# Kernel optimization log

Hardware: AMD Instinct MI355X
Metric: run time of the kernel (lower is better)

## Reference

```python
import jax, jax.numpy as jnp
import numpy as np

N_NODES = 8192
N_EDGES = 65536
NB = 10            # number_of_basis
MID = 32           # middle_layer_size
MAX_R = 10.0       # max_radius
NZ, NM = 48, 16    # z / mol embedding sizes -> 64x0e node input
IN_S = NZ + NM     # 64 scalars
H_S, H_V = 32, 8   # hidden irreps 32x0e + 8x1o (dim 56)
O_S = 16           # output irreps 16x0e
W0N = IN_S * H_S + IN_S * H_V                                  # 2560
W1N = H_S*H_S + H_V*H_S + H_S*H_V + H_V*H_V + H_V*H_V          # 1664
W2N = H_S*O_S + H_V*O_S                                        # 640
H_DIM = H_S + 3 * H_V                                          # 56


def _fcnet(e, W1, W2):
    # e3nn FullyConnectedNet([NB, MID, numel], silu): fan-in normalized linears
    h = jax.nn.silu(e @ W1 / np.sqrt(W1.shape[0]))
    return h @ W2 / np.sqrt(W2.shape[0])


def _ln(x, g, b):
    m = jnp.mean(x, -1, keepdims=True)
    v = jnp.var(x, -1, keepdims=True)
    return (x - m) * jax.lax.rsqrt(v + 1e-5) * g + b


def _sus(t):
    # smooth compact-support bump helper: exp(-1/t) for t>0 else 0
    return jnp.where(t > 0, jnp.exp(-1.0 / jnp.where(t > 0, t, 1.0)), 0.0)


def _forward(pos, Ez, Em,
             b0_W1, b0_W2, b0_g, b0_b,
             b1_W1, b1_W2, b1_g, b1_b,
             b2_W1, b2_W2, b2_g, b2_b,
             z, mol_id, edge_src, edge_dst):
    N = pos.shape[0]
    E = edge_src.shape[0]
    avg = E / N  # avg_num_neighbors (static)

    # node embedding: 64x0e
    x = jnp.concatenate([Ez[z], Em[mol_id]], axis=-1)          # [N, 64]

    vec = pos[edge_dst] - pos[edge_src]                        # [E, 3]
    length = jnp.linalg.norm(vec, axis=1)                      # [E]

    # soft_one_hot_linspace(basis='smooth_finite', cutoff=True) * sqrt(NB)
    vals = jnp.linspace(0.0, MAX_R, NB + 2)[1:-1]
    step = MAX_R / (NB + 1)
    u = (length[:, None] - vals) / step
    emb = (1.14136 * np.exp(2.0)) * _sus(u + 1.0) * _sus(1.0 - u)
    emb = emb * np.sqrt(NB)                                    # [E, NB]

    # spherical harmonics lmax=1, normalize=True, 'component' norm
    nrm = vec / jnp.maximum(length, 1e-9)[:, None]
    sh_v = np.sqrt(3.0) * nrm                                  # [E, 3]  (l=1; l=0 comp == 1)

    # ---- interaction block 0: 64x0e -> 32x0e + 8x1o ----
    w = _fcnet(emb, b0_W1, b0_W2)                              # [E, 2560]
    w00 = w[:, :IN_S * H_S].reshape(E, IN_S, H_S)
    w01 = w[:, IN_S * H_S:].reshape(E, IN_S, H_V)
    xe = x[edge_src]                                           # [E, 64]
    es = jnp.einsum('eu,euw->ew', xe, w00) / np.sqrt(IN_S)
    ev = jnp.einsum('eu,euw,ei->ewi', xe, w01, sh_v) / np.sqrt(IN_S)
    msg = jnp.concatenate([es, ev.reshape(E, 3 * H_V)], -1)    # [E, 56]
    x = _ln(jax.ops.segment_sum(msg, edge_dst, num_segments=N) / np.sqrt(avg), b0_g, b0_b)

    # ---- interaction block 1: 32x0e+8x1o -> 32x0e+8x1o ----
    w = _fcnet(emb, b1_W1, b1_W2)                              # [E, 1664]
    o = 0
    w_ss  = w[:, o:o + H_S*H_S].reshape(E, H_S, H_S); o += H_S*H_S
    w_vvs = w[:, o:o + H_V*H_S].reshape(E, H_V, H_S); o += H_V*H_S
    w_sv  = w[:, o:o + H_S*H_V].reshape(E, H_S, H_V); o += H_S*H_V
    w_vs  = w[:, o:o + H_V*H_V].reshape(E, H_V, H_V); o += H_V*H_V
    w_vvv = w[:, o:o + H_V*H_V].reshape(E, H_V, H_V)
    xs = x[:, :H_S][edge_src]                                  # [E, 32]
    xv = x[:, H_S:].reshape(N, H_V, 3)[edge_src]               # [E, 8, 3]
    dot = jnp.einsum('eui,ei->eu', xv, sh_v) / np.sqrt(3.0)    # 1o x 1o -> 0e CG
    crs = jnp.cross(xv, sh_v[:, None, :]) / np.sqrt(2.0)       # 1o x 1o -> 1o CG
    es = (jnp.einsum('eu,euw->ew', xs, w_ss) / np.sqrt(H_S)
          + jnp.einsum('eu,euw->ew', dot, w_vvs) / np.sqrt(H_V)) / np.sqrt(2.0)
    ev = (jnp.einsum('eu,euw,ei->ewi', xs, w_sv, sh_v) / np.sqrt(H_S)
          + jnp.einsum('eui,euw->ewi', xv, w_vs) / np.sqrt(H_V)
          + jnp.einsum('eui,euw->ewi', crs, w_vvv) / np.sqrt(H_V)) / np.sqrt(3.0)
    msg = jnp.concatenate([es, ev.reshape(E, 3 * H_V)], -1)
    x = _ln(jax.ops.segment_sum(msg, edge_dst, num_segments=N) / np.sqrt(avg), b1_g, b1_b)

    # ---- interaction block 2: 32x0e+8x1o -> 16x0e ----
    w = _fcnet(emb, b2_W1, b2_W2)                              # [E, 640]
    w_ss  = w[:, :H_S * O_S].reshape(E, H_S, O_S)
    w_vvs = w[:, H_S * O_S:].reshape(E, H_V, O_S)
    xs = x[:, :H_S][edge_src]
    xv = x[:, H_S:].reshape(N, H_V, 3)[edge_src]
    dot = jnp.einsum('eui,ei->eu', xv, sh_v) / np.sqrt(3.0)
    es = (jnp.einsum('eu,euw->ew', xs, w_ss) / np.sqrt(H_S)
          + jnp.einsum('eu,euw->ew', dot, w_vvs) / np.sqrt(H_V)) / np.sqrt(2.0)
    x = _ln(jax.ops.segment_sum(es, edge_dst, num_segments=N) / np.sqrt(avg), b2_g, b2_b)
    return x                                                   # [N, 16]


def setup_inputs():
    key = jax.random.key(0)
    ks = jax.random.split(key, 16)
    edge_src = jax.random.randint(ks[3], (N_EDGES,), 0, N_NODES)
    # exclude self-loops (radius_graph never returns them)
    edge_dst = (edge_src + 1 + jax.random.randint(ks[4], (N_EDGES,), 0, N_NODES - 1)) % N_NODES
    return {
        'pos': jax.random.uniform(ks[0], (N_NODES, 3), jnp.float32) * 8.0,
        'z': jax.random.randint(ks[1], (N_NODES,), 0, 100),
        'mol_id': jax.random.randint(ks[2], (N_NODES,), 0, 2),
        'edge_src': edge_src,
        'edge_dst': edge_dst,
        'Ez': jax.random.normal(ks[5], (100, NZ), jnp.float32),
        'Em': jax.random.normal(ks[6], (2, NM), jnp.float32),
        'b0_W1': jax.random.normal(ks[7], (NB, MID), jnp.float32),
        'b0_W2': jax.random.normal(ks[8], (MID, W0N), jnp.float32),
        'b0_g': jnp.ones((H_DIM,), jnp.float32),
        'b0_b': jnp.zeros((H_DIM,), jnp.float32),
        'b1_W1': jax.random.normal(ks[9], (NB, MID), jnp.float32),
        'b1_W2': jax.random.normal(ks[10], (MID, W1N), jnp.float32),
        'b1_g': jnp.ones((H_DIM,), jnp.float32),
        'b1_b': jnp.zeros((H_DIM,), jnp.float32),
        'b2_W1': jax.random.normal(ks[11], (NB, MID), jnp.float32),
        'b2_W2': jax.random.normal(ks[12], (MID, W2N), jnp.float32),
        'b2_g': jnp.ones((O_S,), jnp.float32),
        'b2_b': jnp.zeros((O_S,), jnp.float32),
    }


def reference(pos, z, mol_id, edge_src, edge_dst, Ez, Em,
              b0_W1, b0_W2, b0_g, b0_b,
              b1_W1, b1_W2, b1_g, b1_b,
              b2_W1, b2_W2, b2_g, b2_b):
    return _forward(pos, Ez, Em,
                    b0_W1, b0_W2, b0_g, b0_b,
                    b1_W1, b1_W2, b1_g, b1_b,
                    b2_W1, b2_W2, b2_g, b2_b,
                    z, mol_id, edge_src, edge_dst)
```

## Files before the change

kernel.cpp:

```cpp
#include <hip/hip_runtime.h>

#define NNODES 8192
#define NEDGES 65536

#define K_PACK   0.02209708691f
#define K_P1SV   0.01804219593f
#define K_VVS    0.04419417382f
#define K_VS     0.03608439182f
#define K_VVV    0.02551551815f
#define K_DOT    0.57735026919f
#define K_PRELN  0.35355339059f
#define C_EMB    8.4335730689f

typedef unsigned int uint32;
typedef unsigned short ushort16;
typedef __attribute__((ext_vector_type(8))) short short8;
typedef __attribute__((ext_vector_type(4))) float floatx4;

__device__ __forceinline__ float siluf(float x) { return x / (1.0f + __expf(-x)); }
__device__ __forceinline__ float susf(float t) { return t > 0.0f ? __expf(-1.0f / t) : 0.0f; }
__device__ __forceinline__ ushort16 f2bf(float f) {
  uint32 u = __float_as_uint(f);
  return (ushort16)((u + 0x7fffu + ((u >> 16) & 1u)) >> 16);
}
__device__ __forceinline__ float bflo(uint32 v) { return __uint_as_float(v << 16); }
__device__ __forceinline__ float bfhi(uint32 v) { return __uint_as_float(v & 0xffff0000u); }
__device__ __forceinline__ float bfs(ushort16 v) { return __uint_as_float((uint32)v << 16); }

__device__ __forceinline__ void mlp32(const float* __restrict__ W, const float emb[10],
                                      float* __restrict__ H) {
#pragma unroll
  for (int m = 0; m < 32; ++m) {
    float t = 0.f;
#pragma unroll
    for (int k = 0; k < 10; ++k) t += emb[k] * W[k * 32 + m];
    H[m] = siluf(t);
  }
}

__global__ __launch_bounds__(256) void k_prep(
    const float* __restrict__ pos, const int* __restrict__ z, const int* __restrict__ mol,
    const int* __restrict__ esrc, const int* __restrict__ edst,
    const float* __restrict__ Ez, const float* __restrict__ Em,
    const float* __restrict__ W10, const float* __restrict__ W11, const float* __restrict__ W12,
    const float* __restrict__ W20, const float* __restrict__ W21, const float* __restrict__ W22,
    int* __restrict__ combo, ushort16* __restrict__ X0cb, float* __restrict__ sh,
    ushort16* __restrict__ h0b, ushort16* __restrict__ h1b, ushort16* __restrict__ h2b,
    ushort16* __restrict__ Bp0, ushort16* __restrict__ Bp1, ushort16* __restrict__ Bp2,
    ushort16* __restrict__ Bpw1, ushort16* __restrict__ Bpw2,
    int* __restrict__ deg, int* __restrict__ eidx) {
  int idx = blockIdx.x * 256 + threadIdx.x;
  if (idx < NEDGES) {
    int e = idx;
    int s = esrc[e], d = edst[e];
    int p = atomicAdd(&deg[d], 1);
    if (p < 64) eidx[(size_t)d * 64 + p] = e;
    float vx = pos[d * 3 + 0] - pos[s * 3 + 0];
    float vy = pos[d * 3 + 1] - pos[s * 3 + 1];
    float vz = pos[d * 3 + 2] - pos[s * 3 + 2];
    float len = sqrtf(vx * vx + vy * vy + vz * vz);
    float inv = 1.7320508076f / fmaxf(len, 1e-9f);
    sh[e * 3 + 0] = vx * inv; sh[e * 3 + 1] = vy * inv; sh[e * 3 + 2] = vz * inv;
    float emb[10];
#pragma unroll
    for (int k = 0; k < 10; ++k) {
      float u = len * 1.1f - (float)(k + 1);
      emb[k] = C_EMB * susf(u + 1.0f) * susf(1.0f - u);
    }
    float H[32];
    uint32* hp;
    mlp32(W10, emb, H);
    hp = (uint32*)(h0b + (size_t)e * 32);
#pragma unroll
    for (int m = 0; m < 16; ++m)
      hp[m] = (uint32)f2bf(H[2 * m]) | ((uint32)f2bf(H[2 * m + 1]) << 16);
    mlp32(W11, emb, H);
    hp = (uint32*)(h1b + (size_t)e * 32);
#pragma unroll
    for (int m = 0; m < 16; ++m)
      hp[m] = (uint32)f2bf(H[2 * m]) | ((uint32)f2bf(H[2 * m + 1]) << 16);
    mlp32(W12, emb, H);
    hp = (uint32*)(h2b + (size_t)e * 32);
#pragma unroll
    for (int m = 0; m < 16; ++m)
      hp[m] = (uint32)f2bf(H[2 * m]) | ((uint32)f2bf(H[2 * m + 1]) << 16);
    return;
  }
  idx -= NEDGES;
  if (idx < NNODES) { combo[idx] = z[idx] * 2 + mol[idx]; return; }
  idx -= NNODES;
  if (idx < 16384) {
    int c = idx >> 6, j = idx & 63;
    float v = 0.f;
    if (c < 200) {
      int zz = c >> 1, mm = c & 1;
      v = (j < 48) ? Ez[zz * 48 + j] : Em[mm * 16 + (j - 48)];
    }
    X0cb[idx] = f2bf(v);
    return;
  }
  idx -= 16384;
  if (idx < 81920) {
    int tile = idx >> 10; int r = idx & 1023;
    int kh = r >> 9; int rr = r & 511;
    int lane = rr >> 3, j = rr & 7;
    int k = kh * 32 + (lane >> 4) * 8 + j;
    int n = tile * 16 + (lane & 15);
    int c = n >> 5, m = n & 31;
    int col = (c < 32) ? (k * 32 + c) : (2048 + k * 8 + (c - 32));
    Bp0[idx] = f2bf(W20[m * 2560 + col] * K_PACK);
    return;
  }
  idx -= 81920;
  if (idx < 40960) {
    int tile = idx >> 9; int rr = idx & 511;
    int lane = rr >> 3, j = rr & 7;
    int k = (lane >> 4) * 8 + j;
    int n = tile * 16 + (lane & 15);
    int c = n >> 5, m = n & 31;
    float v = (c < 32) ? W21[m * 1664 + k * 32 + c] * K_PACK
                       : W21[m * 1664 + 1280 + k * 8 + (c - 32)] * K_P1SV;
    Bp1[idx] = f2bf(v);
    return;
  }
  idx -= 40960;
  if (idx < 16384) {
    int tile = idx >> 9; int rr = idx & 511;
    int lane = rr >> 3, j = rr & 7;
    int k = (lane >> 4) * 8 + j;
    int n = tile * 16 + (lane & 15);
    int c = n >> 5, m = n & 31;
    Bp2[idx] = f2bf(W22[m * 640 + k * 16 + c] * K_PACK);
    return;
  }
  idx -= 16384;
  if (idx < 12288) {
    int tile = idx >> 9; int rr = idx & 511;
    int lane = rr >> 3, j = rr & 7;
    int m = (lane >> 4) * 8 + j;
    int c = tile * 16 + (lane & 15);
    float v;
    if (c < 256) {
      int u = c >> 5, w = c & 31;
      v = W21[m * 1664 + 1024 + u * 32 + w] * K_VVS;
    } else {
      int r2 = c - 256; int t = r2 & 1; int l2 = r2 >> 1;
      int u = l2 >> 3, vv = l2 & 7;
      v = (t == 0) ? W21[m * 1664 + 1536 + u * 8 + vv] * K_VS
                   : W21[m * 1664 + 1600 + u * 8 + vv] * K_VVV;
    }
    Bpw1[idx] = f2bf(v);
    return;
  }
  idx -= 12288;
  {
    int tile = idx >> 9; int rr = idx & 511;
    int lane = rr >> 3, j = rr & 7;
    int m = (lane >> 4) * 8 + j;
    int c = tile * 16 + (lane & 15);
    int t = c & 1; int l2 = c >> 1;
    int u = l2 >> 3, wh = l2 & 7;
    Bpw2[idx] = f2bf(W22[m * 640 + 512 + u * 16 + wh * 2 + t] * K_VVS);
  }
}

__device__ __forceinline__ void gemm_tile(
    const ushort16* __restrict__ A, const ushort16* __restrict__ Bp, ushort16* __restrict__ C,
    int N, int K, int bx, int by, int wave, int lane) {
  int m0 = bx * 64 + wave * 16;
  int n0 = by * 64;
  int row = lane & 15, q = lane >> 4;
  int nkh = K >> 5;
  floatx4 acc[4];
  floatx4 zero = {0.f, 0.f, 0.f, 0.f};
#pragma unroll
  for (int t = 0; t < 4; ++t) acc[t] = zero;
  for (int kh = 0; kh < nkh; ++kh) {
    short8 a = *reinterpret_cast<const short8*>(A + (size_t)(m0 + row) * K + kh * 32 + q * 8);
#pragma unroll
    for (int t = 0; t < 4; ++t) {
      int T = (n0 >> 4) + t;
      short8 b = *reinterpret_cast<const short8*>(Bp + ((size_t)T * nkh + kh) * 512 + lane * 8);
      acc[t] = __builtin_amdgcn_mfma_f32_16x16x32_bf16(a, b, acc[t], 0, 0, 0);
    }
  }
  int colb = n0 + row;
#pragma unroll
  for (int t = 0; t < 4; ++t)
#pragma unroll
    for (int r = 0; r < 4; ++r)
      C[(size_t)(m0 + q * 4 + r) * N + colb + t * 16] = f2bf(acc[t][r]);
}

__global__ __launch_bounds__(256) void k_gemm_mfma(
    const ushort16* __restrict__ A, const ushort16* __restrict__ Bp, ushort16* __restrict__ C,
    int N, int K) {
  gemm_tile(A, Bp, C, N, K, blockIdx.x, blockIdx.y, threadIdx.x >> 6, threadIdx.x & 63);
}

__global__ __launch_bounds__(256) void k_gemm3(
    const ushort16* __restrict__ A0, const ushort16* __restrict__ B0, ushort16* __restrict__ C0,
    int N0, int K0, int nbx0, int nb0,
    const ushort16* __restrict__ A1, const ushort16* __restrict__ B1, ushort16* __restrict__ C1,
    int N1, int K1, int nbx1, int nb1,
    const ushort16* __restrict__ A2, const ushort16* __restrict__ B2, ushort16* __restrict__ C2,
    int N2, int K2, int nbx2) {
  int b = blockIdx.x;
  int wave = threadIdx.x >> 6, lane = threadIdx.x & 63;
  if (b < nb0) {
    gemm_tile(A0, B0, C0, N0, K0, b % nbx0, b / nbx0, wave, lane);
  } else if (b < nb0 + nb1) {
    b -= nb0;
    gemm_tile(A1, B1, C1, N1, K1, b % nbx1, b / nbx1, wave, lane);
  } else {
    b -= nb0 + nb1;
    gemm_tile(A2, B2, C2, N2, K2, b % nbx2, b / nbx2, wave, lane);
  }
}

__global__ __launch_bounds__(256) void k_msg0(
    const int* __restrict__ rowmap, const int* __restrict__ esrc,
    const float* __restrict__ sh, const ushort16* __restrict__ hb,
    const ushort16* __restrict__ Pb, ushort16* __restrict__ msg) {
  int e = __builtin_amdgcn_readfirstlane(blockIdx.x * 4 + (threadIdx.x >> 6));
  int lane = threadIdx.x & 63;
  int s = esrc[e];
  int row = rowmap[s];
  float sh0 = sh[e * 3 + 0], sh1 = sh[e * 3 + 1], sh2 = sh[e * 3 + 2];
  int c; float mult;
  if (lane < 32) { c = lane; mult = 1.0f; }
  else if (lane < 56) {
    int l = lane - 32; int v = l / 3; int i = l - v * 3;
    c = 32 + v;
    mult = (i == 0) ? sh0 : (i == 1 ? sh1 : sh2);
  } else { c = 0; mult = 0.0f; }
  const uint4* Hp = reinterpret_cast<const uint4*>(hb + (size_t)e * 32);
  const uint4* Pp = reinterpret_cast<const uint4*>(Pb + (size_t)row * 1280 + c * 32);
  float a = 0.f;
#pragma unroll
  for (int qq = 0; qq < 4; ++qq) {
    uint4 pv = Pp[qq];
    uint4 hv = Hp[qq];
    a += bflo(pv.x) * bflo(hv.x) + bfhi(pv.x) * bfhi(hv.x);
    a += bflo(pv.y) * bflo(hv.y) + bfhi(pv.y) * bfhi(hv.y);
    a += bflo(pv.z) * bflo(hv.z) + bfhi(pv.z) * bfhi(hv.z);
    a += bflo(pv.w) * bflo(hv.w) + bfhi(pv.w) * bfhi(hv.w);
  }
  if (lane < 56) msg[(size_t)e * 56 + lane] = f2bf(a * mult);
}

__global__ __launch_bounds__(256) void k_msg1(
    const int* __restrict__ esrc, const float* __restrict__ sh, const ushort16* __restrict__ hb,
    const ushort16* __restrict__ Pb, const float* __restrict__ xv,
    const ushort16* __restrict__ Wedge, ushort16* __restrict__ msg) {
  __shared__ float vbuf[4][56];
  int w = threadIdx.x >> 6;
  int e = __builtin_amdgcn_readfirstlane(blockIdx.x * 4 + w);
  int lane = threadIdx.x & 63;
  int s = esrc[e];
  float sh0 = sh[e * 3 + 0], sh1 = sh[e * 3 + 1], sh2 = sh[e * 3 + 2];
  int u = lane >> 3;
  const float* xvp = xv + (size_t)s * 24 + u * 3;
  float x0 = xvp[0], x1 = xvp[1], x2 = xvp[2];
  float du = K_DOT * (x0 * sh0 + x1 * sh1 + x2 * sh2);
  float cr0 = x1 * sh2 - x2 * sh1;
  float cr1 = x2 * sh0 - x0 * sh2;
  float cr2 = x0 * sh1 - x1 * sh0;
  const ushort16* wp = Wedge + (size_t)e * 384;
  uint2 wv = *reinterpret_cast<const uint2*>(wp + lane * 4);
  uint32 wsv = *reinterpret_cast<const uint32*>(wp + 256 + lane * 2);
  float b0 = du * bflo(wv.x), b1 = du * bfhi(wv.x);
  float b2 = du * bflo(wv.y), b3 = du * bfhi(wv.y);
  float avs = bflo(wsv), avv = bfhi(wsv);
  float e0v = x0 * avs + cr0 * avv;
  float e1v = x1 * avs + cr1 * avv;
  float e2v = x2 * avs + cr2 * avv;
#pragma unroll
  for (int off = 8; off < 64; off <<= 1) {
    b0 += __shfl_xor(b0, off, 64); b1 += __shfl_xor(b1, off, 64);
    b2 += __shfl_xor(b2, off, 64); b3 += __shfl_xor(b3, off, 64);
    e0v += __shfl_xor(e0v, off, 64); e1v += __shfl_xor(e1v, off, 64);
    e2v += __shfl_xor(e2v, off, 64);
  }
  if (lane < 8) {
    vbuf[w][lane * 4 + 0] = b0; vbuf[w][lane * 4 + 1] = b1;
    vbuf[w][lane * 4 + 2] = b2; vbuf[w][lane * 4 + 3] = b3;
    vbuf[w][32 + lane * 3 + 0] = e0v;
    vbuf[w][32 + lane * 3 + 1] = e1v;
    vbuf[w][32 + lane * 3 + 2] = e2v;
  }
  int c; float mult;
  if (lane < 32) { c = lane; mult = 1.0f; }
  else if (lane < 56) {
    int l = lane - 32; int v = l / 3; int i = l - v * 3;
    c = 32 + v;
    mult = (i == 0) ? sh0 : (i == 1 ? sh1 : sh2);
  } else { c = 0; mult = 0.0f; }
  const uint4* Hp = reinterpret_cast<const uint4*>(hb + (size_t)e * 32);
  const uint4* Pp = reinterpret_cast<const uint4*>(Pb + (size_t)s * 1280 + c * 32);
  float a = 0.f;
#pragma unroll
  for (int qq = 0; qq < 4; ++qq) {
    uint4 pv = Pp[qq];
    uint4 hv = Hp[qq];
    a += bflo(pv.x) * bflo(hv.x) + bfhi(pv.x) * bfhi(hv.x);
    a += bflo(pv.y) * bflo(hv.y) + bfhi(pv.y) * bfhi(hv.y);
    a += bflo(pv.z) * bflo(hv.z) + bfhi(pv.z) * bfhi(hv.z);
    a += bflo(pv.w) * bflo(hv.w) + bfhi(pv.w) * bfhi(hv.w);
  }
  __syncthreads();
  if (lane < 56) msg[(size_t)e * 56 + lane] = f2bf(a * mult + vbuf[w][lane]);
}

__global__ __launch_bounds__(256) void k_msg2(
    const int* __restrict__ esrc, const float* __restrict__ sh, const ushort16* __restrict__ hb,
    const ushort16* __restrict__ Pb, const float* __restrict__ xv,
    const ushort16* __restrict__ Wedge, ushort16* __restrict__ msg) {
  __shared__ float vbuf[4][16];
  int w = threadIdx.x >> 6;
  int e = __builtin_amdgcn_readfirstlane(blockIdx.x * 4 + w);
  int lane = threadIdx.x & 63;
  int s = esrc[e];
  float sh0 = sh[e * 3 + 0], sh1 = sh[e * 3 + 1], sh2 = sh[e * 3 + 2];
  int u = lane >> 3;
  const float* xvp = xv + (size_t)s * 24 + u * 3;
  float du = K_DOT * (xvp[0] * sh0 + xvp[1] * sh1 + xvp[2] * sh2);
  uint32 w2 = *reinterpret_cast<const uint32*>(Wedge + (size_t)e * 128 + lane * 2);
  float c0 = du * bflo(w2), c1 = du * bfhi(w2);
#pragma unroll
  for (int off = 8; off < 64; off <<= 1) {
    c0 += __shfl_xor(c0, off, 64); c1 += __shfl_xor(c1, off, 64);
  }
  if (lane < 8) { vbuf[w][lane * 2 + 0] = c0; vbuf[w][lane * 2 + 1] = c1; }
  int q = lane >> 4, wc = lane & 15;
  uint4 hv = reinterpret_cast<const uint4*>(hb + (size_t)e * 32)[q];
  uint4 pv = reinterpret_cast<const uint4*>(Pb + (size_t)s * 512 + wc * 32)[q];
  float a = bflo(pv.x) * bflo(hv.x) + bfhi(pv.x) * bfhi(hv.x)
          + bflo(pv.y) * bflo(hv.y) + bfhi(pv.y) * bfhi(hv.y)
          + bflo(pv.z) * bflo(hv.z) + bfhi(pv.z) * bfhi(hv.z)
          + bflo(pv.w) * bflo(hv.w) + bfhi(pv.w) * bfhi(hv.w);
  a += __shfl_xor(a, 16, 64);
  a += __shfl_xor(a, 32, 64);
  __syncthreads();
  if (lane < 16) msg[(size_t)e * 16 + lane] = f2bf(a + vbuf[w][lane]);
}

__global__ __launch_bounds__(256) void k_gather_ln(
    const int* __restrict__ deg, const int* __restrict__ eidx,
    const ushort16* __restrict__ msg, int D,
    const float* __restrict__ g, const float* __restrict__ b,
    ushort16* __restrict__ xsb, float* __restrict__ xvf, float* __restrict__ outf) {
  int n = __builtin_amdgcn_readfirstlane(blockIdx.x * 4 + (threadIdx.x >> 6));
  int lane = threadIdx.x & 63;
  int cnt = deg[n]; if (cnt > 64) cnt = 64;
  const int* ep = eidx + (size_t)n * 64;
  float v = 0.f;
  for (int j = 0; j < cnt; ++j) {
    int e = ep[j];
    if (lane < D) v += bfs(msg[(size_t)e * D + lane]);
  }
  v *= K_PRELN;
  if (lane >= D) v = 0.f;
  float sm = v, sq = v * v;
#pragma unroll
  for (int off = 32; off > 0; off >>= 1) {
    sm += __shfl_xor(sm, off, 64);
    sq += __shfl_xor(sq, off, 64);
  }
  float invD = 1.0f / (float)D;
  float mean = sm * invD;
  float var = sq * invD - mean * mean;
  float rs = rsqrtf(var + 1e-5f);
  float r = (v - mean) * rs * g[lane < D ? lane : 0] + b[lane < D ? lane : 0];
  if (outf) {
    if (lane < D) outf[(size_t)n * D + lane] = r;
  } else {
    if (lane < 32) xsb[(size_t)n * 32 + lane] = f2bf(r);
    else if (lane < 56) xvf[(size_t)n * 24 + lane - 32] = r;
  }
}

extern "C" void kernel_launch(void* const* d_in, const int* in_sizes, int n_in,
                              void* d_out, int out_size, void* d_ws, size_t ws_size,
                              hipStream_t stream) {
  const float* pos = (const float*)d_in[0];
  const int* z = (const int*)d_in[1];
  const int* mol = (const int*)d_in[2];
  const int* esrc = (const int*)d_in[3];
  const int* edst = (const int*)d_in[4];
  const float* Ez = (const float*)d_in[5];
  const float* Em = (const float*)d_in[6];
  const float* b0W1 = (const float*)d_in[7];
  const float* b0W2 = (const float*)d_in[8];
  const float* b0g = (const float*)d_in[9];
  const float* b0b = (const float*)d_in[10];
  const float* b1W1 = (const float*)d_in[11];
  const float* b1W2 = (const float*)d_in[12];
  const float* b1g = (const float*)d_in[13];
  const float* b1b = (const float*)d_in[14];
  const float* b2W1 = (const float*)d_in[15];
  const float* b2W2 = (const float*)d_in[16];
  const float* b2g = (const float*)d_in[17];
  const float* b2b = (const float*)d_in[18];
  float* out = (float*)d_out;

  float* ws = (float*)d_ws;
  size_t o = 0;
  int* combo = (int*)(ws + o); o += NNODES;
  int* deg = (int*)(ws + o); o += NNODES;
  int* eidx = (int*)(ws + o); o += (size_t)NNODES * 64;
  ushort16* X0cb = (ushort16*)(ws + o); o += 8192;
  ushort16* xs1b = (ushort16*)(ws + o); o += 131072;
  float* xv1 = ws + o; o += (size_t)NNODES * 24;
  ushort16* h0b = (ushort16*)(ws + o); o += (size_t)NEDGES * 16;
  ushort16* h1b = (ushort16*)(ws + o); o += (size_t)NEDGES * 16;
  ushort16* h2b = (ushort16*)(ws + o); o += (size_t)NEDGES * 16;
  float* shb = ws + o; o += (size_t)NEDGES * 3;
  ushort16* Bp0 = (ushort16*)(ws + o); o += 40960;
  ushort16* Bp1 = (ushort16*)(ws + o); o += 20480;
  ushort16* Bp2 = (ushort16*)(ws + o); o += 8192;
  ushort16* Bpw1 = (ushort16*)(ws + o); o += 6144;
  ushort16* Bpw2 = (ushort16*)(ws + o); o += 2048;
  ushort16* Wedge1 = (ushort16*)(ws + o); o += (size_t)NEDGES * 192;
  ushort16* Wedge2 = (ushort16*)(ws + o); o += (size_t)NEDGES * 64;
  ushort16* P12 = (ushort16*)(ws + o); o += (size_t)NNODES * 640;
  ushort16* msgb = (ushort16*)(ws + o); o += (size_t)NEDGES * 28;

  ushort16* P0c = P12;
  ushort16* xs2b = xs1b;
  float* xv2 = xv1;
  ushort16* msg16 = msgb;

  hipMemsetAsync(deg, 0, NNODES * sizeof(int), stream);

  k_prep<<<960, 256, 0, stream>>>(pos, z, mol, esrc, edst, Ez, Em,
                                  b0W1, b1W1, b2W1, b0W2, b1W2, b2W2,
                                  combo, X0cb, shb, h0b, h1b, h2b,
                                  Bp0, Bp1, Bp2, Bpw1, Bpw2, deg, eidx);

  k_gemm3<<<8272, 256, 0, stream>>>(h1b, Bpw1, Wedge1, 384, 32, 1024, 6144,
                                    h2b, Bpw2, Wedge2, 128, 32, 1024, 2048,
                                    X0cb, Bp0, P0c, 1280, 64, 4);

  k_msg0<<<16384, 256, 0, stream>>>(combo, esrc, shb, h0b, P0c, msgb);
  k_gather_ln<<<2048, 256, 0, stream>>>(deg, eidx, msgb, 56, b0g, b0b, xs1b, xv1, nullptr);

  k_gemm_mfma<<<dim3(128, 20), 256, 0, stream>>>(xs1b, Bp1, P12, 1280, 32);
  k_msg1<<<16384, 256, 0, stream>>>(esrc, shb, h1b, P12, xv1, Wedge1, msgb);
  k_gather_ln<<<2048, 256, 0, stream>>>(deg, eidx, msgb, 56, b1g, b1b, xs2b, xv2, nullptr);

  k_gemm_mfma<<<dim3(128, 8), 256, 0, stream>>>(xs2b, Bp2, P12, 512, 32);
  k_msg2<<<16384, 256, 0, stream>>>(esrc, shb, h2b, P12, xv2, Wedge2, msg16);
  k_gather_ln<<<2048, 256, 0, stream>>>(deg, eidx, msg16, 16, b2g, b2b, nullptr, nullptr, out);
}
```

Before: 245.9 us.

## Fuse per-edge weight GEMMs into message kernels via MFMA into LDS

```diff
diff --git a/kernel.cpp b/kernel.cpp
--- a/kernel.cpp
+++ b/kernel.cpp
@@ -198,26 +198,6 @@
   gemm_tile(A, Bp, C, N, K, blockIdx.x, blockIdx.y, threadIdx.x >> 6, threadIdx.x & 63);
 }
 
-__global__ __launch_bounds__(256) void k_gemm3(
-    const ushort16* __restrict__ A0, const ushort16* __restrict__ B0, ushort16* __restrict__ C0,
-    int N0, int K0, int nbx0, int nb0,
-    const ushort16* __restrict__ A1, const ushort16* __restrict__ B1, ushort16* __restrict__ C1,
-    int N1, int K1, int nbx1, int nb1,
-    const ushort16* __restrict__ A2, const ushort16* __restrict__ B2, ushort16* __restrict__ C2,
-    int N2, int K2, int nbx2) {
-  int b = blockIdx.x;
-  int wave = threadIdx.x >> 6, lane = threadIdx.x & 63;
-  if (b < nb0) {
-    gemm_tile(A0, B0, C0, N0, K0, b % nbx0, b / nbx0, wave, lane);
-  } else if (b < nb0 + nb1) {
-    b -= nb0;
-    gemm_tile(A1, B1, C1, N1, K1, b % nbx1, b / nbx1, wave, lane);
-  } else {
-    b -= nb0 + nb1;
-    gemm_tile(A2, B2, C2, N2, K2, b % nbx2, b / nbx2, wave, lane);
-  }
-}
-
 __global__ __launch_bounds__(256) void k_msg0(
     const int* __restrict__ rowmap, const int* __restrict__ esrc,
     const float* __restrict__ sh, const ushort16* __restrict__ hb,
@@ -249,100 +229,134 @@
   if (lane < 56) msg[(size_t)e * 56 + lane] = f2bf(a * mult);
 }
 
-__global__ __launch_bounds__(256) void k_msg1(
+__global__ __launch_bounds__(256) void k_msg1f(
     const int* __restrict__ esrc, const float* __restrict__ sh, const ushort16* __restrict__ hb,
     const ushort16* __restrict__ Pb, const float* __restrict__ xv,
-    const ushort16* __restrict__ Wedge, ushort16* __restrict__ msg) {
+    const ushort16* __restrict__ Bpw, ushort16* __restrict__ msg) {
+  __shared__ ushort16 Wlds[16][384];
   __shared__ float vbuf[4][56];
-  int w = threadIdx.x >> 6;
-  int e = __builtin_amdgcn_readfirstlane(blockIdx.x * 4 + w);
-  int lane = threadIdx.x & 63;
-  int s = esrc[e];
-  float sh0 = sh[e * 3 + 0], sh1 = sh[e * 3 + 1], sh2 = sh[e * 3 + 2];
+  int w = threadIdx.x >> 6, lane = threadIdx.x & 63;
+  int e0 = __builtin_amdgcn_readfirstlane(blockIdx.x * 16);
+  int row = lane & 15, q = lane >> 4;
+  short8 a1 = *reinterpret_cast<const short8*>(hb + (size_t)(e0 + row) * 32 + q * 8);
+  floatx4 zero = {0.f, 0.f, 0.f, 0.f};
+#pragma unroll
+  for (int t6 = 0; t6 < 6; ++t6) {
+    int T = w * 6 + t6;
+    short8 b1 = *reinterpret_cast<const short8*>(Bpw + (size_t)T * 512 + lane * 8);
+    floatx4 acc = __builtin_amdgcn_mfma_f32_16x16x32_bf16(a1, b1, zero, 0, 0, 0);
+#pragma unroll
+    for (int r = 0; r < 4; ++r)
+      Wlds[q * 4 + r][T * 16 + row] = f2bf(acc[r]);
+  }
+  __syncthreads();
   int u = lane >> 3;
-  const float* xvp = xv + (size_t)s * 24 + u * 3;
-  float x0 = xvp[0], x1 = xvp[1], x2 = xvp[2];
-  float du = K_DOT * (x0 * sh0 + x1 * sh1 + x2 * sh2);
-  float cr0 = x1 * sh2 - x2 * sh1;
-  float cr1 = x2 * sh0 - x0 * sh2;
-  float cr2 = x0 * sh1 - x1 * sh0;
-  const ushort16* wp = Wedge + (size_t)e * 384;
-  uint2 wv = *reinterpret_cast<const uint2*>(wp + lane * 4);
-  uint32 wsv = *reinterpret_cast<const uint32*>(wp + 256 + lane * 2);
-  float b0 = du * bflo(wv.x), b1 = du * bfhi(wv.x);
-  float b2 = du * bflo(wv.y), b3 = du * bfhi(wv.y);
-  float avs = bflo(wsv), avv = bfhi(wsv);
-  float e0v = x0 * avs + cr0 * avv;
-  float e1v = x1 * avs + cr1 * avv;
-  float e2v = x2 * avs + cr2 * avv;
-#pragma unroll
-  for (int off = 8; off < 64; off <<= 1) {
-    b0 += __shfl_xor(b0, off, 64); b1 += __shfl_xor(b1, off, 64);
-    b2 += __shfl_xor(b2, off, 64); b3 += __shfl_xor(b3, off, 64);
-    e0v += __shfl_xor(e0v, off, 64); e1v += __shfl_xor(e1v, off, 64);
-    e2v += __shfl_xor(e2v, off, 64);
-  }
-  if (lane < 8) {
-    vbuf[w][lane * 4 + 0] = b0; vbuf[w][lane * 4 + 1] = b1;
-    vbuf[w][lane * 4 + 2] = b2; vbuf[w][lane * 4 + 3] = b3;
-    vbuf[w][32 + lane * 3 + 0] = e0v;
-    vbuf[w][32 + lane * 3 + 1] = e1v;
-    vbuf[w][32 + lane * 3 + 2] = e2v;
-  }
-  int c; float mult;
-  if (lane < 32) { c = lane; mult = 1.0f; }
-  else if (lane < 56) {
-    int l = lane - 32; int v = l / 3; int i = l - v * 3;
-    c = 32 + v;
-    mult = (i == 0) ? sh0 : (i == 1 ? sh1 : sh2);
-  } else { c = 0; mult = 0.0f; }
-  const uint4* Hp = reinterpret_cast<const uint4*>(hb + (size_t)e * 32);
-  const uint4* Pp = reinterpret_cast<const uint4*>(Pb + (size_t)s * 1280 + c * 32);
-  float a = 0.f;
-#pragma unroll
-  for (int qq = 0; qq < 4; ++qq) {
-    uint4 pv = Pp[qq];
-    uint4 hv = Hp[qq];
-    a += bflo(pv.x) * bflo(hv.x) + bfhi(pv.x) * bfhi(hv.x);
-    a += bflo(pv.y) * bflo(hv.y) + bfhi(pv.y) * bfhi(hv.y);
-    a += bflo(pv.z) * bflo(hv.z) + bfhi(pv.z) * bfhi(hv.z);
-    a += bflo(pv.w) * bflo(hv.w) + bfhi(pv.w) * bfhi(hv.w);
-  }
-  __syncthreads();
-  if (lane < 56) msg[(size_t)e * 56 + lane] = f2bf(a * mult + vbuf[w][lane]);
-}
-
-__global__ __launch_bounds__(256) void k_msg2(
+#pragma unroll
+  for (int k = 0; k < 4; ++k) {
+    int e = e0 + w * 4 + k;
+    int s = esrc[e];
+    float sh0 = sh[e * 3 + 0], sh1 = sh[e * 3 + 1], sh2 = sh[e * 3 + 2];
+    const float* xvp = xv + (size_t)s * 24 + u * 3;
+    float x0 = xvp[0], x1 = xvp[1], x2 = xvp[2];
+    float du = K_DOT * (x0 * sh0 + x1 * sh1 + x2 * sh2);
+    float cr0 = x1 * sh2 - x2 * sh1;
+    float cr1 = x2 * sh0 - x0 * sh2;
+    float cr2 = x0 * sh1 - x1 * sh0;
+    const ushort16* wp = &Wlds[w * 4 + k][0];
+    uint2 wv = *reinterpret_cast<const uint2*>(wp + lane * 4);
+    uint32 wsv = *reinterpret_cast<const uint32*>(wp + 256 + lane * 2);
+    float b0 = du * bflo(wv.x), b1 = du * bfhi(wv.x);
+    float b2 = du * bflo(wv.y), b3 = du * bfhi(wv.y);
+    float avs = bflo(wsv), avv = bfhi(wsv);
+    float e0v = x0 * avs + cr0 * avv;
+    float e1v = x1 * avs + cr1 * avv;
+    float e2v = x2 * avs + cr2 * avv;
+#pragma unroll
+    for (int off = 8; off < 64; off <<= 1) {
+      b0 += __shfl_xor(b0, off, 64); b1 += __shfl_xor(b1, off, 64);
+      b2 += __shfl_xor(b2, off, 64); b3 += __shfl_xor(b3, off, 64);
+      e0v += __shfl_xor(e0v, off, 64); e1v += __shfl_xor(e1v, off, 64);
+      e2v += __shfl_xor(e2v, off, 64);
+    }
+    if (lane < 8) {
+      vbuf[w][lane * 4 + 0] = b0; vbuf[w][lane * 4 + 1] = b1;
+      vbuf[w][lane * 4 + 2] = b2; vbuf[w][lane * 4 + 3] = b3;
+      vbuf[w][32 + lane * 3 + 0] = e0v;
+      vbuf[w][32 + lane * 3 + 1] = e1v;
+      vbuf[w][32 + lane * 3 + 2] = e2v;
+    }
+    int c; float mult;
+    if (lane < 32) { c = lane; mult = 1.0f; }
+    else if (lane < 56) {
+      int l = lane - 32; int v = l / 3; int i = l - v * 3;
+      c = 32 + v;
+      mult = (i == 0) ? sh0 : (i == 1 ? sh1 : sh2);
+    } else { c = 0; mult = 0.0f; }
+    const uint4* Hp = reinterpret_cast<const uint4*>(hb + (size_t)e * 32);
+    const uint4* Pp = reinterpret_cast<const uint4*>(Pb + (size_t)s * 1280 + c * 32);
+    float a = 0.f;
+#pragma unroll
+    for (int qq = 0; qq < 4; ++qq) {
+      uint4 pv = Pp[qq];
+      uint4 hv = Hp[qq];
+      a += bflo(pv.x) * bflo(hv.x) + bfhi(pv.x) * bfhi(hv.x);
+      a += bflo(pv.y) * bflo(hv.y) + bfhi(pv.y) * bfhi(hv.y);
+      a += bflo(pv.z) * bflo(hv.z) + bfhi(pv.z) * bfhi(hv.z);
+      a += bflo(pv.w) * bflo(hv.w) + bfhi(pv.w) * bfhi(hv.w);
+    }
+    __syncthreads();
+    if (lane < 56) msg[(size_t)e * 56 + lane] = f2bf(a * mult + vbuf[w][lane]);
+  }
+}
+
+__global__ __launch_bounds__(256) void k_msg2f(
     const int* __restrict__ esrc, const float* __restrict__ sh, const ushort16* __restrict__ hb,
     const ushort16* __restrict__ Pb, const float* __restrict__ xv,
-    const ushort16* __restrict__ Wedge, ushort16* __restrict__ msg) {
+    const ushort16* __restrict__ Bpw, ushort16* __restrict__ msg) {
+  __shared__ ushort16 Wlds[16][128];
   __shared__ float vbuf[4][16];
-  int w = threadIdx.x >> 6;
-  int e = __builtin_amdgcn_readfirstlane(blockIdx.x * 4 + w);
-  int lane = threadIdx.x & 63;
-  int s = esrc[e];
-  float sh0 = sh[e * 3 + 0], sh1 = sh[e * 3 + 1], sh2 = sh[e * 3 + 2];
+  int w = threadIdx.x >> 6, lane = threadIdx.x & 63;
+  int e0 = __builtin_amdgcn_readfirstlane(blockIdx.x * 16);
+  int row = lane & 15, q = lane >> 4;
+  short8 a1 = *reinterpret_cast<const short8*>(hb + (size_t)(e0 + row) * 32 + q * 8);
+  floatx4 zero = {0.f, 0.f, 0.f, 0.f};
+#pragma unroll
+  for (int t2 = 0; t2 < 2; ++t2) {
+    int T = w * 2 + t2;
+    short8 b1 = *reinterpret_cast<const short8*>(Bpw + (size_t)T * 512 + lane * 8);
+    floatx4 acc = __builtin_amdgcn_mfma_f32_16x16x32_bf16(a1, b1, zero, 0, 0, 0);
+#pragma unroll
+    for (int r = 0; r < 4; ++r)
+      Wlds[q * 4 + r][T * 16 + row] = f2bf(acc[r]);
+  }
+  __syncthreads();
   int u = lane >> 3;
-  const float* xvp = xv + (size_t)s * 24 + u * 3;
-  float du = K_DOT * (xvp[0] * sh0 + xvp[1] * sh1 + xvp[2] * sh2);
-  uint32 w2 = *reinterpret_cast<const uint32*>(Wedge + (size_t)e * 128 + lane * 2);
-  float c0 = du * bflo(w2), c1 = du * bfhi(w2);
-#pragma unroll
-  for (int off = 8; off < 64; off <<= 1) {
-    c0 += __shfl_xor(c0, off, 64); c1 += __shfl_xor(c1, off, 64);
-  }
-  if (lane < 8) { vbuf[w][lane * 2 + 0] = c0; vbuf[w][lane * 2 + 1] = c1; }
-  int q = lane >> 4, wc = lane & 15;
-  uint4 hv = reinterpret_cast<const uint4*>(hb + (size_t)e * 32)[q];
-  uint4 pv = reinterpret_cast<const uint4*>(Pb + (size_t)s * 512 + wc * 32)[q];
-  float a = bflo(pv.x) * bflo(hv.x) + bfhi(pv.x) * bfhi(hv.x)
-          + bflo(pv.y) * bflo(hv.y) + bfhi(pv.y) * bfhi(hv.y)
-          + bflo(pv.z) * bflo(hv.z) + bfhi(pv.z) * bfhi(hv.z)
-          + bflo(pv.w) * bflo(hv.w) + bfhi(pv.w) * bfhi(hv.w);
-  a += __shfl_xor(a, 16, 64);
-  a += __shfl_xor(a, 32, 64);
-  __syncthreads();
-  if (lane < 16) msg[(size_t)e * 16 + lane] = f2bf(a + vbuf[w][lane]);
+#pragma unroll
+  for (int k = 0; k < 4; ++k) {
+    int e = e0 + w * 4 + k;
+    int s = esrc[e];
+    float sh0 = sh[e * 3 + 0], sh1 = sh[e * 3 + 1], sh2 = sh[e * 3 + 2];
+    const float* xvp = xv + (size_t)s * 24 + u * 3;
+    float du = K_DOT * (xvp[0] * sh0 + xvp[1] * sh1 + xvp[2] * sh2);
+    uint32 w2 = *reinterpret_cast<const uint32*>(&Wlds[w * 4 + k][0] + lane * 2);
+    float c0 = du * bflo(w2), c1 = du * bfhi(w2);
+#pragma unroll
+    for (int off = 8; off < 64; off <<= 1) {
+      c0 += __shfl_xor(c0, off, 64); c1 += __shfl_xor(c1, off, 64);
+    }
+    if (lane < 8) { vbuf[w][lane * 2 + 0] = c0; vbuf[w][lane * 2 + 1] = c1; }
+    int qq = lane >> 4, wc = lane & 15;
+    uint4 hv = reinterpret_cast<const uint4*>(hb + (size_t)e * 32)[qq];
+    uint4 pv = reinterpret_cast<const uint4*>(Pb + (size_t)s * 512 + wc * 32)[qq];
+    float a = bflo(pv.x) * bflo(hv.x) + bfhi(pv.x) * bfhi(hv.x)
+            + bflo(pv.y) * bflo(hv.y) + bfhi(pv.y) * bfhi(hv.y)
+            + bflo(pv.z) * bflo(hv.z) + bfhi(pv.z) * bfhi(hv.z)
+            + bflo(pv.w) * bflo(hv.w) + bfhi(pv.w) * bfhi(hv.w);
+    a += __shfl_xor(a, 16, 64);
+    a += __shfl_xor(a, 32, 64);
+    __syncthreads();
+    if (lane < 16) msg[(size_t)e * 16 + lane] = f2bf(a + vbuf[w][lane]);
+  }
 }
 
 __global__ __launch_bounds__(256) void k_gather_ln(
@@ -421,8 +435,6 @@
   ushort16* Bp2 = (ushort16*)(ws + o); o += 8192;
   ushort16* Bpw1 = (ushort16*)(ws + o); o += 6144;
   ushort16* Bpw2 = (ushort16*)(ws + o); o += 2048;
-  ushort16* Wedge1 = (ushort16*)(ws + o); o += (size_t)NEDGES * 192;
-  ushort16* Wedge2 = (ushort16*)(ws + o); o += (size_t)NEDGES * 64;
   ushort16* P12 = (ushort16*)(ws + o); o += (size_t)NNODES * 640;
   ushort16* msgb = (ushort16*)(ws + o); o += (size_t)NEDGES * 28;
 
@@ -438,18 +450,15 @@
                                   combo, X0cb, shb, h0b, h1b, h2b,
                                   Bp0, Bp1, Bp2, Bpw1, Bpw2, deg, eidx);
 
-  k_gemm3<<<8272, 256, 0, stream>>>(h1b, Bpw1, Wedge1, 384, 32, 1024, 6144,
-                                    h2b, Bpw2, Wedge2, 128, 32, 1024, 2048,
-                                    X0cb, Bp0, P0c, 1280, 64, 4);
-
+  k_gemm_mfma<<<dim3(4, 20), 256, 0, stream>>>(X0cb, Bp0, P0c, 1280, 64);
   k_msg0<<<16384, 256, 0, stream>>>(combo, esrc, shb, h0b, P0c, msgb);
   k_gather_ln<<<2048, 256, 0, stream>>>(deg, eidx, msgb, 56, b0g, b0b, xs1b, xv1, nullptr);
 
   k_gemm_mfma<<<dim3(128, 20), 256, 0, stream>>>(xs1b, Bp1, P12, 1280, 32);
-  k_msg1<<<16384, 256, 0, stream>>>(esrc, shb, h1b, P12, xv1, Wedge1, msgb);
+  k_msg1f<<<4096, 256, 0, stream>>>(esrc, shb, h1b, P12, xv1, Bpw1, msgb);
   k_gather_ln<<<2048, 256, 0, stream>>>(deg, eidx, msgb, 56, b1g, b1b, xs2b, xv2, nullptr);
 
   k_gemm_mfma<<<dim3(128, 8), 256, 0, stream>>>(xs2b, Bp2, P12, 512, 32);
-  k_msg2<<<16384, 256, 0, stream>>>(esrc, shb, h2b, P12, xv2, Wedge2, msg16);
+  k_msg2f<<<4096, 256, 0, stream>>>(esrc, shb, h2b, P12, xv2, Bpw2, msg16);
   k_gather_ln<<<2048, 256, 0, stream>>>(deg, eidx, msg16, 16, b2g, b2b, nullptr, nullptr, out);
 }
```

Result: no change. 247.2 us (+0.6%).
